# Performance work log

Measured on AMD Instinct MI355X. Metric: run time of the kernel, lower is better.

## Reference

```python
import jax, jax.numpy as jnp
import numpy as np
from jax import lax

ANCHOR_BASE = np.array([
    [-37.254833, -82.50967, 53.254833, 98.50967],
    [-82.50967, -173.01933, 98.50967, 189.01933],
    [-173.01933, -354.03867, 189.01933, 370.03867],
    [-56.0, -56.0, 72.0, 72.0],
    [-120.0, -120.0, 136.0, 136.0],
    [-248.0, -248.0, 264.0, 264.0],
    [-82.50967, -37.254833, 98.50967, 53.254833],
    [-173.01933, -82.50967, 189.01933, 98.50967],
    [-354.03867, -173.01933, 370.03867, 189.01933]], dtype=np.float32)
FEAT_STRIDE = 16
IMG_H, IMG_W = 608, 800          # feature map 38x50 at stride 16
NMS_THRESH = 0.7
PRE_NMS, POST_NMS = 6000, 300
MIN_SIZE = 16.0                  # scale = 1.0


def setup_inputs() -> dict:
    key = jax.random.key(0)
    ks = jax.random.split(key, 7)
    H, W = 38, 50
    x = jax.random.normal(ks[0], (1, 512, H, W), jnp.float32)
    conv1_w = jax.random.normal(ks[1], (512, 512, 3, 3), jnp.float32) * 0.01
    conv1_b = jnp.zeros((512,), jnp.float32)
    loc_w = jax.random.normal(ks[2], (36, 512, 1, 1), jnp.float32) * 0.01
    loc_b = jnp.zeros((36,), jnp.float32)
    score_w = jax.random.normal(ks[3], (18, 512, 1, 1), jnp.float32) * 0.01
    score_b = jnp.zeros((18,), jnp.float32)
    return {"x": x, "conv1_w": conv1_w, "conv1_b": conv1_b,
            "loc_w": loc_w, "loc_b": loc_b,
            "score_w": score_w, "score_b": score_b}


def _conv(x, w, b, pad):
    y = lax.conv_general_dilated(x, w, (1, 1), pad,
                                 dimension_numbers=("NCHW", "OIHW", "NCHW"))
    return y + b[None, :, None, None]


def _make_anchors(h, w):
    ab = jnp.asarray(ANCHOR_BASE)                       # [A,4]
    yy = jnp.arange(h, dtype=jnp.float32) * FEAT_STRIDE
    xx = jnp.arange(w, dtype=jnp.float32) * FEAT_STRIDE
    sy, sx = jnp.meshgrid(yy, xx, indexing="ij")        # [h,w]
    shift = jnp.stack([sy, sx, sy, sx], axis=-1).reshape(-1, 4)  # [K,4]
    return (shift[:, None, :] + ab[None, :, :]).reshape(-1, 4)   # [K*A,4]


def _loc2bbox(anchor, loc):
    ah = anchor[:, 2] - anchor[:, 0]
    aw = anchor[:, 3] - anchor[:, 1]
    acy = anchor[:, 0] + 0.5 * ah
    acx = anchor[:, 1] + 0.5 * aw
    dy, dx, dh, dw = loc[:, 0], loc[:, 1], loc[:, 2], loc[:, 3]
    cy = dy * ah + acy
    cx = dx * aw + acx
    h = jnp.exp(dh) * ah
    w = jnp.exp(dw) * aw
    return jnp.stack([cy - 0.5 * h, cx - 0.5 * w,
                      cy + 0.5 * h, cx + 0.5 * w], axis=1)


def _iou_matrix(b):  # b: [K,4] (y1,x1,y2,x2)
    area = (b[:, 2] - b[:, 0]) * (b[:, 3] - b[:, 1])
    ty1 = jnp.maximum(b[:, None, 0], b[None, :, 0])
    tx1 = jnp.maximum(b[:, None, 1], b[None, :, 1])
    ty2 = jnp.minimum(b[:, None, 2], b[None, :, 2])
    tx2 = jnp.minimum(b[:, None, 3], b[None, :, 3])
    inter = jnp.clip(ty2 - ty1, 0) * jnp.clip(tx2 - tx1, 0)
    return inter / jnp.maximum(area[:, None] + area[None, :] - inter, 1e-9)


def _nms_keep(boxes, valid, thresh):
    # boxes already sorted by score desc; greedy suppression.
    K = boxes.shape[0]
    iou = _iou_matrix(boxes)                 # [K,K]
    idx = jnp.arange(K)

    def body(i, keep):
        sup = (iou[i] > thresh) & (idx > i) & keep[i]
        return keep & ~sup

    keep = lax.fori_loop(0, K, body, valid)
    return keep


def reference(x, conv1_w, conv1_b, loc_w, loc_b, score_w, score_b):
    H, W = x.shape[2], x.shape[3]
    A = ANCHOR_BASE.shape[0]

    h1 = jax.nn.relu(_conv(x, conv1_w, conv1_b, ((1, 1), (1, 1))))
    locs = _conv(h1, loc_w, loc_b, ((0, 0), (0, 0)))      # [1,36,H,W]
    scores = _conv(h1, score_w, score_b, ((0, 0), (0, 0)))  # [1,18,H,W]

    locs = locs.transpose(0, 2, 3, 1).reshape(-1, 4)        # [H*W*A,4]
    fg = scores.transpose(0, 2, 3, 1).reshape(H, W, A, 2)[..., 1].reshape(-1)

    anchor = _make_anchors(H, W)
    roi = _loc2bbox(anchor, locs)
    roi = jnp.stack([jnp.clip(roi[:, 0], 0, IMG_H),
                     jnp.clip(roi[:, 1], 0, IMG_W),
                     jnp.clip(roi[:, 2], 0, IMG_H),
                     jnp.clip(roi[:, 3], 0, IMG_W)], axis=1)

    hs = roi[:, 2] - roi[:, 0]
    ws = roi[:, 3] - roi[:, 1]
    valid = (hs >= MIN_SIZE) & (ws >= MIN_SIZE)
    score_f = jnp.where(valid, fg, -jnp.inf)

    top_scores, top_idx = lax.top_k(score_f, PRE_NMS)
    top_boxes = roi[top_idx]                                # [PRE_NMS,4]
    top_valid = top_scores > -jnp.inf

    keep = _nms_keep(top_boxes, top_valid, NMS_THRESH)

    # take first POST_NMS kept boxes into a fixed-shape output
    rank = jnp.cumsum(keep.astype(jnp.int32)) - 1
    dest = jnp.where(keep & (rank < POST_NMS), rank, POST_NMS)
    out = jnp.zeros((POST_NMS + 1, 4), top_boxes.dtype).at[dest].add(top_boxes)
    return out[:POST_NMS]
```

## Files before the change

kernel.cpp:

```cpp
#include <hip/hip_runtime.h>
#include <cstdint>
#include <cstddef>

typedef unsigned long long u64;

#define CIN   512
#define H     38
#define W     50
#define HW    1900
#define PH    40
#define PW    52
#define NA    17100
#define NSORT 32768
#define PRE   6000
#define POST  300
#define NW    94
#define MTS   6016
#define TOPN  6016

__constant__ float c_AB[36] = {
  -37.254833f,  -82.50967f,   53.254833f,  98.50967f,
  -82.50967f,  -173.01933f,   98.50967f,  189.01933f,
 -173.01933f,  -354.03867f,  189.01933f,  370.03867f,
  -56.f, -56.f, 72.f, 72.f,
 -120.f,-120.f,136.f,136.f,
 -248.f,-248.f,264.f,264.f,
  -82.50967f,  -37.254833f,   98.50967f,  53.254833f,
 -173.01933f,  -82.50967f,   189.01933f,  98.50967f,
 -354.03867f, -173.01933f,   370.03867f, 189.01933f
};

__global__ __launch_bounds__(256) void pad_kernel(const float* __restrict__ x, float* __restrict__ xp) {
  int idx = blockIdx.x * 256 + threadIdx.x;
  int c   = idx / (PH * PW);
  int rem = idx - c * (PH * PW);
  int yy  = rem / PW;
  int xx  = rem - yy * PW;
  float v = 0.f;
  if (yy >= 1 && yy <= H && xx >= 1 && xx <= W)
    v = x[(size_t)c * HW + (yy - 1) * W + (xx - 1)];
  xp[idx] = v;
}

__global__ __launch_bounds__(256) void wtrans_kernel(const float* __restrict__ w1, float* __restrict__ wt) {
  __shared__ float tile[9][16][17];
  int o0 = blockIdx.x * 16, i0 = blockIdx.y * 16;
  int tx = threadIdx.x & 15, ty = threadIdx.x >> 4;
  #pragma unroll
  for (int r = 0; r < 9; ++r)
    tile[r][tx][ty] = w1[((size_t)(o0 + ty) * CIN + (i0 + tx)) * 9 + r];
  __syncthreads();
  #pragma unroll
  for (int r = 0; r < 9; ++r)
    wt[((size_t)r * CIN + i0 + ty) * CIN + o0 + tx] = tile[r][ty][tx];
}

__global__ __launch_bounds__(256) void wt2prep_kernel(const float* __restrict__ lw, const float* __restrict__ sw,
                                                      float* __restrict__ wt2) {
  int t = blockIdx.x * 256 + threadIdx.x;
  int k = t >> 6, o = t & 63;
  float v = 0.f;
  if (o < 36)      v = lw[o * CIN + k];
  else if (o < 54) v = sw[(o - 36) * CIN + k];
  wt2[t] = v;
}

__global__ __launch_bounds__(256) void conv_gemm_kernel(const float* __restrict__ wt, const float* __restrict__ xp,
                                                        float* __restrict__ part) {
  __shared__ __align__(16) float As[16][64];
  __shared__ __align__(16) float Bs[16][64];
  const int tid   = threadIdx.x;
  const int obase = blockIdx.x * 64;
  const int pbase = blockIdx.y * 64;
  const int split = blockIdx.z;
  const int kbeg = split * 1536, kend = kbeg + 1536;
  const int krow = tid >> 4;
  const int c4   = (tid & 15) * 4;
  const int to   = (tid & 15) * 4;
  const int tp   = (tid >> 4) * 4;
  float acc[4][4] = {};
  float av[4], bv[4];

  auto loadAB = [&](int k0) {
    int k = k0 + krow;
    const float* ap = &wt[(size_t)k * CIN + obase + c4];
    av[0] = ap[0]; av[1] = ap[1]; av[2] = ap[2]; av[3] = ap[3];
    int r = k >> 9;
    int i = k & 511;
    int ky = r / 3, kx = r - ky * 3;
    const float* xpi = &xp[(size_t)i * (PH * PW)];
    #pragma unroll
    for (int j = 0; j < 4; ++j) {
      int p = pbase + c4 + j;
      float v = 0.f;
      if (p < HW) {
        int y = p / W, xx = p - y * W;
        v = xpi[(y + ky) * PW + xx + kx];
      }
      bv[j] = v;
    }
  };

  loadAB(kbeg);
  for (int k0 = kbeg; k0 < kend; k0 += 16) {
    __syncthreads();
    *(float4*)&As[krow][c4] = make_float4(av[0], av[1], av[2], av[3]);
    *(float4*)&Bs[krow][c4] = make_float4(bv[0], bv[1], bv[2], bv[3]);
    __syncthreads();
    if (k0 + 16 < kend) loadAB(k0 + 16);
    #pragma unroll
    for (int kk = 0; kk < 16; ++kk) {
      float4 a4 = *(const float4*)&As[kk][to];
      float4 b4 = *(const float4*)&Bs[kk][tp];
      float ar[4] = {a4.x, a4.y, a4.z, a4.w};
      float br[4] = {b4.x, b4.y, b4.z, b4.w};
      #pragma unroll
      for (int ii = 0; ii < 4; ++ii)
        #pragma unroll
        for (int jj = 0; jj < 4; ++jj)
          acc[ii][jj] += ar[ii] * br[jj];
    }
  }
  float* dst = part + (size_t)split * CIN * HW;
  #pragma unroll
  for (int ii = 0; ii < 4; ++ii) {
    int o = obase + to + ii;
    int p = pbase + tp;
    float* rowp = dst + (size_t)o * HW;
    if (p + 3 < HW) {
      *(float4*)&rowp[p] = make_float4(acc[ii][0], acc[ii][1], acc[ii][2], acc[ii][3]);
    } else {
      #pragma unroll
      for (int jj = 0; jj < 4; ++jj) if (p + jj < HW) rowp[p + jj] = acc[ii][jj];
    }
  }
}

__global__ __launch_bounds__(256) void reduce_relu_kernel(const float* __restrict__ part, const float* __restrict__ b1,
                                                          float* __restrict__ h1) {
  int idx = blockIdx.x * 256 + threadIdx.x;
  int o = idx / HW;
  float v = part[idx] + part[(size_t)CIN * HW + idx] + part[(size_t)2 * CIN * HW + idx] + b1[o];
  h1[idx] = v > 0.f ? v : 0.f;
}

__global__ __launch_bounds__(256) void heads_gemm_kernel(const float* __restrict__ wt2, const float* __restrict__ h1,
                                                         const float* __restrict__ lb, const float* __restrict__ sb,
                                                         float* __restrict__ c2) {
  __shared__ __align__(16) float As[16][64];
  __shared__ __align__(16) float Bs[16][64];
  const int tid   = threadIdx.x;
  const int pbase = blockIdx.x * 64;
  const int krow = tid >> 4;
  const int c4   = (tid & 15) * 4;
  const int to   = (tid & 15) * 4;
  const int tp   = (tid >> 4) * 4;
  float acc[4][4] = {};
  float av[4], bv[4];

  auto loadAB = [&](int k0) {
    int k = k0 + krow;
    const float4 a4 = *(const float4*)&wt2[k * 64 + c4];
    av[0] = a4.x; av[1] = a4.y; av[2] = a4.z; av[3] = a4.w;
    #pragma unroll
    for (int j = 0; j < 4; ++j) {
      int p = pbase + c4 + j;
      bv[j] = (p < HW) ? h1[(size_t)k * HW + p] : 0.f;
    }
  };

  loadAB(0);
  for (int k0 = 0; k0 < CIN; k0 += 16) {
    __syncthreads();
    *(float4*)&As[krow][c4] = make_float4(av[0], av[1], av[2], av[3]);
    *(float4*)&Bs[krow][c4] = make_float4(bv[0], bv[1], bv[2], bv[3]);
    __syncthreads();
    if (k0 + 16 < CIN) loadAB(k0 + 16);
    #pragma unroll
    for (int kk = 0; kk < 16; ++kk) {
      float4 a4 = *(const float4*)&As[kk][to];
      float4 b4 = *(const float4*)&Bs[kk][tp];
      float ar[4] = {a4.x, a4.y, a4.z, a4.w};
      float br[4] = {b4.x, b4.y, b4.z, b4.w};
      #pragma unroll
      for (int ii = 0; ii < 4; ++ii)
        #pragma unroll
        for (int jj = 0; jj < 4; ++jj)
          acc[ii][jj] += ar[ii] * br[jj];
    }
  }
  #pragma unroll
  for (int ii = 0; ii < 4; ++ii) {
    int o = to + ii;
    float bias = 0.f;
    if (o < 36) bias = lb[o]; else if (o < 54) bias = sb[o - 36];
    int p = pbase + tp;
    float* rowp = c2 + (size_t)o * HW;
    #pragma unroll
    for (int jj = 0; jj < 4; ++jj) if (p + jj < HW) rowp[p + jj] = acc[ii][jj] + bias;
  }
}

__global__ __launch_bounds__(256) void decode_kernel(const float* __restrict__ c2, float* __restrict__ roi,
                                                     u64* __restrict__ keys) {
  int n = blockIdx.x * 256 + threadIdx.x;
  if (n >= NSORT) return;
  if (n >= NA) { keys[n] = ~0ull; return; }
  unsigned p = (unsigned)n / 9u;
  unsigned a = (unsigned)n - p * 9u;
  unsigned y = p / 50u;
  unsigned x = p - y * 50u;
  float dy = c2[(a * 4 + 0) * HW + p];
  float dx = c2[(a * 4 + 1) * HW + p];
  float dh = c2[(a * 4 + 2) * HW + p];
  float dw = c2[(a * 4 + 3) * HW + p];
  float fg = c2[(37 + a * 2) * HW + p];
  float sy = (float)(y * 16u), sx = (float)(x * 16u);
  float ay1 = sy + c_AB[a * 4 + 0], ax1 = sx + c_AB[a * 4 + 1];
  float ay2 = sy + c_AB[a * 4 + 2], ax2 = sx + c_AB[a * 4 + 3];
  float ahh = ay2 - ay1, aww = ax2 - ax1;
  float acy = ay1 + 0.5f * ahh, acx = ax1 + 0.5f * aww;
  float cy = dy * ahh + acy, cx = dx * aww + acx;
  float hh = expf(dh) * ahh, ww = expf(dw) * aww;
  float y1 = cy - 0.5f * hh, x1 = cx - 0.5f * ww;
  float y2 = cy + 0.5f * hh, x2 = cx + 0.5f * ww;
  y1 = fminf(fmaxf(y1, 0.f), 608.f); x1 = fminf(fmaxf(x1, 0.f), 800.f);
  y2 = fminf(fmaxf(y2, 0.f), 608.f); x2 = fminf(fmaxf(x2, 0.f), 800.f);
  *(float4*)&roi[(size_t)n * 4] = make_float4(y1, x1, y2, x2);
  bool valid = ((y2 - y1) >= 16.f) && ((x2 - x1) >= 16.f);
  float sc = valid ? fg : -__builtin_huge_valf();
  unsigned m = __float_as_uint(sc);
  m = (m & 0x80000000u) ? ~m : (m | 0x80000000u);
  unsigned km = ~m;
  keys[n] = ((u64)km << 32) | (unsigned)n;
}

__global__ __launch_bounds__(256) void sortchunk_kernel(u64* __restrict__ keys) {
  __shared__ u64 s[2048];
  const int tid = threadIdx.x;
  u64* base = keys + (size_t)blockIdx.x * 2048;
  for (int i = tid; i < 2048; i += 256) s[i] = base[i];
  __syncthreads();
  for (int k = 2; k <= 2048; k <<= 1) {
    for (int j = k >> 1; j > 0; j >>= 1) {
      for (int i = tid; i < 2048; i += 256) {
        int l = i ^ j;
        if (l > i) {
          u64 xa = s[i], xb = s[l];
          bool up = ((i & k) == 0);
          if ((xa > xb) == up) { s[i] = xb; s[l] = xa; }
        }
      }
      __syncthreads();
    }
  }
  for (int i = tid; i < 2048; i += 256) base[i] = s[i];
}

__device__ inline void merge_path(const u64* __restrict__ A, int nA, const u64* __restrict__ B, int nB,
                                  u64* __restrict__ dst, int d0, int cnt, int outLimit) {
  if (d0 >= outLimit || d0 >= nA + nB) return;
  int lo = d0 > nB ? d0 - nB : 0;
  int hi = d0 < nA ? d0 : nA;
  while (lo < hi) {
    int mid = (lo + hi) >> 1;
    if (A[mid] <= B[d0 - 1 - mid]) lo = mid + 1; else hi = mid;
  }
  int i = lo, j = d0 - lo;
  int end = d0 + cnt;
  if (end > nA + nB) end = nA + nB;
  if (end > outLimit) end = outLimit;
  for (int q = d0; q < end; ++q) {
    u64 v;
    if (i < nA && (j >= nB || A[i] <= B[j])) v = A[i++]; else v = B[j++];
    dst[q] = v;
  }
}

__global__ __launch_bounds__(256) void merge4_kernel(const u64* __restrict__ keys, u64* __restrict__ tmp) {
  __shared__ u64 M01[4096];
  __shared__ u64 M23[4096];
  const int tid = threadIdx.x;
  const u64* c = keys + (size_t)blockIdx.x * 8192;
  merge_path(c,        2048, c + 2048, 2048, M01, tid * 16, 16, 4096);
  merge_path(c + 4096, 2048, c + 6144, 2048, M23, tid * 16, 16, 4096);
  __syncthreads();
  merge_path(M01, 4096, M23, 4096, tmp + (size_t)blockIdx.x * TOPN, tid * 24, 24, TOPN);
}

__global__ __launch_bounds__(256) void mergefinal_kernel(const u64* __restrict__ tmp, u64* __restrict__ topk) {
  __shared__ u64 L0[TOPN];
  __shared__ u64 L1[TOPN];
  const int tid = threadIdx.x;
  merge_path(tmp,            TOPN, tmp + TOPN,     TOPN, L0, tid * 24, 24, TOPN);
  merge_path(tmp + 2 * TOPN, TOPN, tmp + 3 * TOPN, TOPN, L1, tid * 24, 24, TOPN);
  __syncthreads();
  merge_path(L0, TOPN, L1, TOPN, topk, tid * 24, 24, TOPN);
}

__global__ __launch_bounds__(256) void gather_kernel(const u64* __restrict__ topk, const float* __restrict__ roi,
                                                     float* __restrict__ tb, float* __restrict__ areaArr,
                                                     u64* __restrict__ valw) {
  int j = blockIdx.x * 256 + threadIdx.x;
  u64 key = (j < TOPN) ? topk[j] : ~0ull;
  bool valid = (j < PRE) && ((unsigned)(key >> 32) < 0xFF800000u);
  if (j < PRE) {
    unsigned idx = (unsigned)key;
    float4 b = *(const float4*)&roi[(size_t)idx * 4];
    *(float4*)&tb[(size_t)j * 4] = b;
    areaArr[j] = (b.z - b.x) * (b.w - b.y);
  }
  u64 mask = __ballot(valid);
  if ((threadIdx.x & 63) == 0) {
    int wi = j >> 6;
    if (wi < NW) valw[wi] = mask;
  }
}

__global__ __launch_bounds__(256) void mask_kernel(const float* __restrict__ tb, const float* __restrict__ areaArr,
                                                   u64* __restrict__ MT) {
  int linear = blockIdx.x * 256 + threadIdx.x;
  if (linear >= NW * PRE) return;
  int w = linear / PRE;
  int i = linear - w * PRE;
  u64 bits = 0;
  int jbase = w * 64;
  if (jbase + 63 > i) {
    float4 bi = *(const float4*)&tb[(size_t)i * 4];
    float ai = areaArr[i];
    int jend = jbase + 64; if (jend > PRE) jend = PRE;
    int jst = jbase > i + 1 ? jbase : i + 1;
    for (int j = jst; j < jend; ++j) {
      float4 bj = *(const float4*)&tb[(size_t)j * 4];
      float ty1 = fmaxf(bi.x, bj.x);
      float tx1 = fmaxf(bi.y, bj.y);
      float ty2 = fminf(bi.z, bj.z);
      float tx2 = fminf(bi.w, bj.w);
      float ih = ty2 - ty1; if (ih < 0.f) ih = 0.f;
      float iw = tx2 - tx1; if (iw < 0.f) iw = 0.f;
      float inter = ih * iw;
      float denom = ai + areaArr[j] - inter;
      if (denom < 1e-9f) denom = 1e-9f;
      if (inter / denom > 0.7f) bits |= (1ull << (j - jbase));
    }
  }
  MT[(size_t)w * MTS + i] = bits;
}

__device__ inline u64 shfl_u64(u64 v, int src) {
  int lo = __shfl((int)(unsigned)(v & 0xffffffffull), src, 64);
  int hi = __shfl((int)(unsigned)(v >> 32), src, 64);
  return ((u64)(unsigned)hi << 32) | (unsigned)lo;
}

__global__ __launch_bounds__(64) void nms_scan_kernel(const u64* __restrict__ MT, const u64* __restrict__ valw,
                                                      const float* __restrict__ tb, float* __restrict__ out) {
  __shared__ u64 removed[NW];
  __shared__ int keepids[POST];
  const int lane = threadIdx.x;
  for (int wk = lane; wk < NW; wk += 64) removed[wk] = 0;
  __syncthreads();
  int kept = 0;
  bool done = false;
  for (int g = 0; g < NW && !done; ++g) {
    int row = g * 64 + lane;
    u64 cur = (row < PRE) ? MT[(size_t)g * MTS + row] : 0ull;
    u64 v = valw[g];
    u64 r = removed[g];
    u64 kb = 0;
    u64 remaining = v & ~r;
    while (remaining) {
      int c = __builtin_ctzll(remaining);
      if (lane == 0) keepids[kept] = g * 64 + c;
      kb |= (1ull << c);
      ++kept;
      if (kept >= POST) { done = true; break; }
      u64 cw = shfl_u64(cur, c);
      r |= cw;
      u64 above = (c == 63) ? 0ull : (~0ull << (c + 1));
      remaining = v & ~r & above;
    }
    if (!done) {
      __syncthreads();
      for (int wk = g + 1 + lane; wk < NW; wk += 64) {
        u64 acc2 = removed[wk];
        u64 m = kb;
        while (m) {
          int b = __builtin_ctzll(m); m &= m - 1;
          acc2 |= MT[(size_t)wk * MTS + g * 64 + b];
        }
        removed[wk] = acc2;
      }
      __syncthreads();
    }
  }
  __syncthreads();
  int kmax = kept < POST ? kept : POST;
  for (int rr = lane; rr < kmax; rr += 64) {
    float4 b = *(const float4*)&tb[(size_t)keepids[rr] * 4];
    *(float4*)&out[(size_t)rr * 4] = b;
  }
}

extern "C" void kernel_launch(void* const* d_in, const int* in_sizes, int n_in,
                              void* d_out, int out_size, void* d_ws, size_t ws_size,
                              hipStream_t stream) {
  (void)in_sizes; (void)n_in; (void)ws_size;
  const float* x  = (const float*)d_in[0];
  const float* w1 = (const float*)d_in[1];
  const float* b1 = (const float*)d_in[2];
  const float* lw = (const float*)d_in[3];
  const float* lb = (const float*)d_in[4];
  const float* sw = (const float*)d_in[5];
  const float* sb = (const float*)d_in[6];
  float* out = (float*)d_out;

  char* wp = (char*)d_ws;
  auto alloc = [&](size_t b) -> void* { void* p = wp; wp += (b + 255) & ~(size_t)255; return p; };
  float* xp      = (float*)alloc((size_t)CIN * PH * PW * 4);
  float* wt      = (float*)alloc((size_t)4608 * CIN * 4);
  float* part    = (float*)alloc((size_t)3 * CIN * HW * 4);
  float* h1      = (float*)alloc((size_t)CIN * HW * 4);
  float* wt2     = (float*)alloc((size_t)CIN * 64 * 4);
  float* c2      = (float*)alloc((size_t)64 * HW * 4);
  float* roi     = (float*)alloc((size_t)NA * 4 * 4);
  u64*   keys    = (u64*)alloc((size_t)NSORT * 8);
  u64*   tmp     = (u64*)alloc((size_t)NSORT * 8);
  u64*   topk    = (u64*)alloc((size_t)8192 * 8);
  float* tb      = (float*)alloc((size_t)PRE * 4 * 4);
  float* areaArr = (float*)alloc((size_t)PRE * 4);
  u64*   valw    = (u64*)alloc((size_t)NW * 8);
  u64*   MT      = (u64*)alloc((size_t)NW * MTS * 8);

  hipMemsetAsync(d_out, 0, (size_t)out_size * 4, stream);

  pad_kernel<<<(CIN * PH * PW) / 256, 256, 0, stream>>>(x, xp);
  wtrans_kernel<<<dim3(32, 32), 256, 0, stream>>>(w1, wt);
  wt2prep_kernel<<<(CIN * 64) / 256, 256, 0, stream>>>(lw, sw, wt2);
  conv_gemm_kernel<<<dim3(8, 30, 3), 256, 0, stream>>>(wt, xp, part);
  reduce_relu_kernel<<<(CIN * HW) / 256, 256, 0, stream>>>(part, b1, h1);
  heads_gemm_kernel<<<30, 256, 0, stream>>>(wt2, h1, lb, sb, c2);
  decode_kernel<<<NSORT / 256, 256, 0, stream>>>(c2, roi, keys);
  sortchunk_kernel<<<16, 256, 0, stream>>>(keys);
  merge4_kernel<<<4, 256, 0, stream>>>(keys, tmp);
  mergefinal_kernel<<<1, 256, 0, stream>>>(tmp, topk);
  gather_kernel<<<24, 256, 0, stream>>>(topk, roi, tb, areaArr, valw);
  mask_kernel<<<(NW * PRE + 255) / 256, 256, 0, stream>>>(tb, areaArr, MT);
  nms_scan_kernel<<<1, 64, 0, stream>>>(MT, valw, tb, out);
}
```

Before: 527.7 us.

## Fuse prep kernels, split heads GEMM into per-output dots, rework NMS scan

Merges the padding, weight-transpose and head-weight prep kernels into one launch, and fuses the final merge with the top-k gather. The 30-block heads GEMM becomes a 54x30 grid of 64-thread dot-product blocks reading a transposed weight copy, to raise parallelism. The NMS scan drops the per-group shared-memory update of later columns. Instead it ORs the mask rows of all kept boxes for each group and reduces across the wavefront. This trades fewer launches and syncs for redundant reads of h1 across output channels and a scan cost that grows with the number of kept boxes.

```diff
diff --git a/kernel.cpp b/kernel.cpp
--- a/kernel.cpp
+++ b/kernel.cpp
@@ -30,39 +30,42 @@
  -354.03867f, -173.01933f,   370.03867f, 189.01933f
 };
 
-__global__ __launch_bounds__(256) void pad_kernel(const float* __restrict__ x, float* __restrict__ xp) {
-  int idx = blockIdx.x * 256 + threadIdx.x;
-  int c   = idx / (PH * PW);
-  int rem = idx - c * (PH * PW);
-  int yy  = rem / PW;
-  int xx  = rem - yy * PW;
-  float v = 0.f;
-  if (yy >= 1 && yy <= H && xx >= 1 && xx <= W)
-    v = x[(size_t)c * HW + (yy - 1) * W + (xx - 1)];
-  xp[idx] = v;
-}
-
-__global__ __launch_bounds__(256) void wtrans_kernel(const float* __restrict__ w1, float* __restrict__ wt) {
+__global__ __launch_bounds__(256) void prep_kernel(const float* __restrict__ x, float* __restrict__ xp,
+                                                   const float* __restrict__ w1, float* __restrict__ wt,
+                                                   const float* __restrict__ lw, const float* __restrict__ sw,
+                                                   float* __restrict__ wt2, float* __restrict__ wt2t) {
   __shared__ float tile[9][16][17];
-  int o0 = blockIdx.x * 16, i0 = blockIdx.y * 16;
-  int tx = threadIdx.x & 15, ty = threadIdx.x >> 4;
-  #pragma unroll
-  for (int r = 0; r < 9; ++r)
-    tile[r][tx][ty] = w1[((size_t)(o0 + ty) * CIN + (i0 + tx)) * 9 + r];
-  __syncthreads();
-  #pragma unroll
-  for (int r = 0; r < 9; ++r)
-    wt[((size_t)r * CIN + i0 + ty) * CIN + o0 + tx] = tile[r][ty][tx];
-}
-
-__global__ __launch_bounds__(256) void wt2prep_kernel(const float* __restrict__ lw, const float* __restrict__ sw,
-                                                      float* __restrict__ wt2) {
-  int t = blockIdx.x * 256 + threadIdx.x;
-  int k = t >> 6, o = t & 63;
-  float v = 0.f;
-  if (o < 36)      v = lw[o * CIN + k];
-  else if (o < 54) v = sw[(o - 36) * CIN + k];
-  wt2[t] = v;
+  int b = blockIdx.x;
+  if (b < 4160) {
+    int idx = b * 256 + threadIdx.x;
+    int c   = idx / (PH * PW);
+    int rem = idx - c * (PH * PW);
+    int yy  = rem / PW;
+    int xx  = rem - yy * PW;
+    float v = 0.f;
+    if (yy >= 1 && yy <= H && xx >= 1 && xx <= W)
+      v = x[(size_t)c * HW + (yy - 1) * W + (xx - 1)];
+    xp[idx] = v;
+  } else if (b < 5184) {
+    int t2 = b - 4160;
+    int o0 = (t2 & 31) * 16, i0 = (t2 >> 5) * 16;
+    int tx = threadIdx.x & 15, ty = threadIdx.x >> 4;
+    #pragma unroll
+    for (int r = 0; r < 9; ++r)
+      tile[r][tx][ty] = w1[((size_t)(o0 + ty) * CIN + (i0 + tx)) * 9 + r];
+    __syncthreads();
+    #pragma unroll
+    for (int r = 0; r < 9; ++r)
+      wt[((size_t)r * CIN + i0 + ty) * CIN + o0 + tx] = tile[r][ty][tx];
+  } else {
+    int t = (b - 5184) * 256 + threadIdx.x;
+    int k = t >> 6, o = t & 63;
+    float v = 0.f;
+    if (o < 36)      v = lw[o * CIN + k];
+    else if (o < 54) v = sw[(o - 36) * CIN + k];
+    wt2[t] = v;
+    wt2t[(size_t)o * CIN + k] = v;
+  }
 }
 
 __global__ __launch_bounds__(256) void conv_gemm_kernel(const float* __restrict__ wt, const float* __restrict__ xp,
@@ -144,60 +147,32 @@
   h1[idx] = v > 0.f ? v : 0.f;
 }
 
-__global__ __launch_bounds__(256) void heads_gemm_kernel(const float* __restrict__ wt2, const float* __restrict__ h1,
-                                                         const float* __restrict__ lb, const float* __restrict__ sb,
-                                                         float* __restrict__ c2) {
-  __shared__ __align__(16) float As[16][64];
-  __shared__ __align__(16) float Bs[16][64];
-  const int tid   = threadIdx.x;
-  const int pbase = blockIdx.x * 64;
-  const int krow = tid >> 4;
-  const int c4   = (tid & 15) * 4;
-  const int to   = (tid & 15) * 4;
-  const int tp   = (tid >> 4) * 4;
-  float acc[4][4] = {};
-  float av[4], bv[4];
-
-  auto loadAB = [&](int k0) {
-    int k = k0 + krow;
-    const float4 a4 = *(const float4*)&wt2[k * 64 + c4];
-    av[0] = a4.x; av[1] = a4.y; av[2] = a4.z; av[3] = a4.w;
-    #pragma unroll
-    for (int j = 0; j < 4; ++j) {
-      int p = pbase + c4 + j;
-      bv[j] = (p < HW) ? h1[(size_t)k * HW + p] : 0.f;
-    }
-  };
-
-  loadAB(0);
-  for (int k0 = 0; k0 < CIN; k0 += 16) {
-    __syncthreads();
-    *(float4*)&As[krow][c4] = make_float4(av[0], av[1], av[2], av[3]);
-    *(float4*)&Bs[krow][c4] = make_float4(bv[0], bv[1], bv[2], bv[3]);
-    __syncthreads();
-    if (k0 + 16 < CIN) loadAB(k0 + 16);
-    #pragma unroll
-    for (int kk = 0; kk < 16; ++kk) {
-      float4 a4 = *(const float4*)&As[kk][to];
-      float4 b4 = *(const float4*)&Bs[kk][tp];
-      float ar[4] = {a4.x, a4.y, a4.z, a4.w};
-      float br[4] = {b4.x, b4.y, b4.z, b4.w};
-      #pragma unroll
-      for (int ii = 0; ii < 4; ++ii)
-        #pragma unroll
-        for (int jj = 0; jj < 4; ++jj)
-          acc[ii][jj] += ar[ii] * br[jj];
-    }
-  }
-  #pragma unroll
-  for (int ii = 0; ii < 4; ++ii) {
-    int o = to + ii;
-    float bias = 0.f;
-    if (o < 36) bias = lb[o]; else if (o < 54) bias = sb[o - 36];
-    int p = pbase + tp;
-    float* rowp = c2 + (size_t)o * HW;
-    #pragma unroll
-    for (int jj = 0; jj < 4; ++jj) if (p + jj < HW) rowp[p + jj] = acc[ii][jj] + bias;
+__global__ __launch_bounds__(64) void heads_dot_kernel(const float* __restrict__ wt2t, const float* __restrict__ h1,
+                                                       const float* __restrict__ lb, const float* __restrict__ sb,
+                                                       float* __restrict__ c2) {
+  const int o = blockIdx.x;
+  const int p = blockIdx.y * 64 + threadIdx.x;
+  const bool pv = (p < HW);
+  const float* __restrict__ ap = wt2t + ((size_t)o << 9);
+  const float* __restrict__ bp = h1 + (pv ? p : 0);
+  float acc = 0.f;
+  #pragma unroll 1
+  for (int g = 0; g < CIN; g += 16) {
+    float4 a0 = *(const float4*)(ap + g);
+    float4 a1 = *(const float4*)(ap + g + 4);
+    float4 a2 = *(const float4*)(ap + g + 8);
+    float4 a3 = *(const float4*)(ap + g + 12);
+    float bb[16];
+    #pragma unroll
+    for (int u = 0; u < 16; ++u) bb[u] = bp[(size_t)(g + u) * HW];
+    acc += a0.x * bb[0];  acc += a0.y * bb[1];  acc += a0.z * bb[2];  acc += a0.w * bb[3];
+    acc += a1.x * bb[4];  acc += a1.y * bb[5];  acc += a1.z * bb[6];  acc += a1.w * bb[7];
+    acc += a2.x * bb[8];  acc += a2.y * bb[9];  acc += a2.z * bb[10]; acc += a2.w * bb[11];
+    acc += a3.x * bb[12]; acc += a3.y * bb[13]; acc += a3.z * bb[14]; acc += a3.w * bb[15];
+  }
+  if (pv) {
+    float bias = (o < 36) ? lb[o] : sb[o - 36];
+    c2[(size_t)o * HW + p] = acc + bias;
   }
 }
 
@@ -288,32 +263,34 @@
   merge_path(M01, 4096, M23, 4096, tmp + (size_t)blockIdx.x * TOPN, tid * 24, 24, TOPN);
 }
 
-__global__ __launch_bounds__(256) void mergefinal_kernel(const u64* __restrict__ tmp, u64* __restrict__ topk) {
+__global__ __launch_bounds__(256) void mergefinal_gather_kernel(const u64* __restrict__ tmp,
+                                                                const float* __restrict__ roi,
+                                                                float* __restrict__ tb, float* __restrict__ areaArr,
+                                                                u64* __restrict__ valw) {
   __shared__ u64 L0[TOPN];
   __shared__ u64 L1[TOPN];
+  __shared__ u64 F[TOPN];
   const int tid = threadIdx.x;
   merge_path(tmp,            TOPN, tmp + TOPN,     TOPN, L0, tid * 24, 24, TOPN);
   merge_path(tmp + 2 * TOPN, TOPN, tmp + 3 * TOPN, TOPN, L1, tid * 24, 24, TOPN);
   __syncthreads();
-  merge_path(L0, TOPN, L1, TOPN, topk, tid * 24, 24, TOPN);
-}
-
-__global__ __launch_bounds__(256) void gather_kernel(const u64* __restrict__ topk, const float* __restrict__ roi,
-                                                     float* __restrict__ tb, float* __restrict__ areaArr,
-                                                     u64* __restrict__ valw) {
-  int j = blockIdx.x * 256 + threadIdx.x;
-  u64 key = (j < TOPN) ? topk[j] : ~0ull;
-  bool valid = (j < PRE) && ((unsigned)(key >> 32) < 0xFF800000u);
-  if (j < PRE) {
-    unsigned idx = (unsigned)key;
-    float4 b = *(const float4*)&roi[(size_t)idx * 4];
-    *(float4*)&tb[(size_t)j * 4] = b;
-    areaArr[j] = (b.z - b.x) * (b.w - b.y);
-  }
-  u64 mask = __ballot(valid);
-  if ((threadIdx.x & 63) == 0) {
-    int wi = j >> 6;
-    if (wi < NW) valw[wi] = mask;
+  merge_path(L0, TOPN, L1, TOPN, F, tid * 24, 24, TOPN);
+  __syncthreads();
+  for (int j0 = 0; j0 < TOPN; j0 += 256) {
+    int j = j0 + tid;
+    u64 key = F[j];
+    bool valid = (j < PRE) && ((unsigned)(key >> 32) < 0xFF800000u);
+    if (j < PRE) {
+      unsigned idx = (unsigned)key;
+      float4 bx = *(const float4*)&roi[(size_t)idx * 4];
+      *(float4*)&tb[(size_t)j * 4] = bx;
+      areaArr[j] = (bx.z - bx.x) * (bx.w - bx.y);
+    }
+    u64 mask = __ballot(valid);
+    if ((tid & 63) == 0) {
+      int wi = j >> 6;
+      if (wi < NW) valw[wi] = mask;
+    }
   }
 }
 
@@ -352,46 +329,39 @@
   int hi = __shfl((int)(unsigned)(v >> 32), src, 64);
   return ((u64)(unsigned)hi << 32) | (unsigned)lo;
 }
+__device__ inline u64 shfl_u64_xor(u64 v, int m) {
+  int lo = __shfl_xor((int)(unsigned)(v & 0xffffffffull), m, 64);
+  int hi = __shfl_xor((int)(unsigned)(v >> 32), m, 64);
+  return ((u64)(unsigned)hi << 32) | (unsigned)lo;
+}
 
 __global__ __launch_bounds__(64) void nms_scan_kernel(const u64* __restrict__ MT, const u64* __restrict__ valw,
                                                       const float* __restrict__ tb, float* __restrict__ out) {
-  __shared__ u64 removed[NW];
   __shared__ int keepids[POST];
   const int lane = threadIdx.x;
-  for (int wk = lane; wk < NW; wk += 64) removed[wk] = 0;
-  __syncthreads();
   int kept = 0;
   bool done = false;
   for (int g = 0; g < NW && !done; ++g) {
+    const u64* __restrict__ rowg = MT + (size_t)g * MTS;
+    u64 rem = 0;
+    for (int base = 0; base < kept; base += 64) {
+      int kidx = base + lane;
+      u64 v = (kidx < kept) ? rowg[keepids[kidx]] : 0ull;
+      rem |= v;
+    }
+    #pragma unroll
+    for (int s = 32; s > 0; s >>= 1) rem |= shfl_u64_xor(rem, s);
     int row = g * 64 + lane;
-    u64 cur = (row < PRE) ? MT[(size_t)g * MTS + row] : 0ull;
-    u64 v = valw[g];
-    u64 r = removed[g];
-    u64 kb = 0;
-    u64 remaining = v & ~r;
+    u64 cur = (row < PRE) ? rowg[row] : 0ull;
+    u64 remaining = valw[g] & ~rem;
     while (remaining) {
       int c = __builtin_ctzll(remaining);
       if (lane == 0) keepids[kept] = g * 64 + c;
-      kb |= (1ull << c);
       ++kept;
       if (kept >= POST) { done = true; break; }
       u64 cw = shfl_u64(cur, c);
-      r |= cw;
       u64 above = (c == 63) ? 0ull : (~0ull << (c + 1));
-      remaining = v & ~r & above;
-    }
-    if (!done) {
-      __syncthreads();
-      for (int wk = g + 1 + lane; wk < NW; wk += 64) {
-        u64 acc2 = removed[wk];
-        u64 m = kb;
-        while (m) {
-          int b = __builtin_ctzll(m); m &= m - 1;
-          acc2 |= MT[(size_t)wk * MTS + g * 64 + b];
-        }
-        removed[wk] = acc2;
-      }
-      __syncthreads();
+      remaining = remaining & ~cw & above;
     }
   }
   __syncthreads();
@@ -422,11 +392,11 @@
   float* part    = (float*)alloc((size_t)3 * CIN * HW * 4);
   float* h1      = (float*)alloc((size_t)CIN * HW * 4);
   float* wt2     = (float*)alloc((size_t)CIN * 64 * 4);
+  float* wt2t    = (float*)alloc((size_t)64 * CIN * 4);
   float* c2      = (float*)alloc((size_t)64 * HW * 4);
   float* roi     = (float*)alloc((size_t)NA * 4 * 4);
   u64*   keys    = (u64*)alloc((size_t)NSORT * 8);
   u64*   tmp     = (u64*)alloc((size_t)NSORT * 8);
-  u64*   topk    = (u64*)alloc((size_t)8192 * 8);
   float* tb      = (float*)alloc((size_t)PRE * 4 * 4);
   float* areaArr = (float*)alloc((size_t)PRE * 4);
   u64*   valw    = (u64*)alloc((size_t)NW * 8);
@@ -434,17 +404,14 @@
 
   hipMemsetAsync(d_out, 0, (size_t)out_size * 4, stream);
 
-  pad_kernel<<<(CIN * PH * PW) / 256, 256, 0, stream>>>(x, xp);
-  wtrans_kernel<<<dim3(32, 32), 256, 0, stream>>>(w1, wt);
-  wt2prep_kernel<<<(CIN * 64) / 256, 256, 0, stream>>>(lw, sw, wt2);
+  prep_kernel<<<5312, 256, 0, stream>>>(x, xp, w1, wt, lw, sw, wt2, wt2t);
   conv_gemm_kernel<<<dim3(8, 30, 3), 256, 0, stream>>>(wt, xp, part);
   reduce_relu_kernel<<<(CIN * HW) / 256, 256, 0, stream>>>(part, b1, h1);
-  heads_gemm_kernel<<<30, 256, 0, stream>>>(wt2, h1, lb, sb, c2);
+  heads_dot_kernel<<<dim3(54, 30), 64, 0, stream>>>(wt2t, h1, lb, sb, c2);
   decode_kernel<<<NSORT / 256, 256, 0, stream>>>(c2, roi, keys);
   sortchunk_kernel<<<16, 256, 0, stream>>>(keys);
   merge4_kernel<<<4, 256, 0, stream>>>(keys, tmp);
-  mergefinal_kernel<<<1, 256, 0, stream>>>(tmp, topk);
-  gather_kernel<<<24, 256, 0, stream>>>(topk, roi, tb, areaArr, valw);
+  mergefinal_gather_kernel<<<1, 256, 0, stream>>>(tmp, roi, tb, areaArr, valw);
   mask_kernel<<<(NW * PRE + 255) / 256, 256, 0, stream>>>(tb, areaArr, MT);
   nms_scan_kernel<<<1, 64, 0, stream>>>(MT, valw, tb, out);
 }
```

After: 456.0 us. -13.6%, faster.
